# Performance work log

Hardware: AMD Instinct MI355X
Metric: run time of the kernel (lower is better)

## Reference

```python
import jax, jax.numpy as jnp
import numpy as np
import math

MUL = 32
E = 131072
N = 10000
IRREPS = [(0, 1), (1, -1), (2, 1)]  # (l, parity) for 0e + 1o + 2e
SQRT3 = math.sqrt(3.0)

_f = math.factorial


def _w3j_symbol(j1, j2, j3, m1, m2, m3):
    """Standard (complex-basis) Wigner 3j symbol via the Racah formula."""
    if m1 + m2 + m3 != 0:
        return 0.0
    if abs(m1) > j1 or abs(m2) > j2 or abs(m3) > j3:
        return 0.0
    if not (abs(j1 - j2) <= j3 <= j1 + j2):
        return 0.0
    tri = _f(j1 + j2 - j3) * _f(j1 - j2 + j3) * _f(-j1 + j2 + j3) / _f(j1 + j2 + j3 + 1)
    pref = (-1) ** (j1 - j2 - m3) * math.sqrt(
        tri * _f(j1 + m1) * _f(j1 - m1) * _f(j2 + m2) * _f(j2 - m2) * _f(j3 + m3) * _f(j3 - m3)
    )
    tmin = max(0, j2 - j3 - m1, j1 - j3 + m2)
    tmax = min(j1 + j2 - j3, j1 - m1, j2 + m2)
    s = 0.0
    for t in range(tmin, tmax + 1):
        s += (-1) ** t / (
            _f(t) * _f(j3 - j2 + t + m1) * _f(j3 - j1 + t - m2)
            * _f(j1 + j2 - j3 - t) * _f(j1 - t - m1) * _f(j2 - t + m2)
        )
    return pref * s


def _real_basis(l):
    """Complex -> real spherical-harmonic change of basis, rows m=-l..l."""
    U = np.zeros((2 * l + 1, 2 * l + 1), dtype=np.complex128)
    U[l, l] = 1.0
    s = 1.0 / math.sqrt(2.0)
    for m in range(1, l + 1):
        U[l + m, l + m] = ((-1) ** m) * s
        U[l + m, l - m] = s
        U[l - m, l - m] = 1j * s
        U[l - m, l + m] = -1j * ((-1) ** m) * s
    return U


def _w3j_real(l1, l2, l3):
    """Real-basis Wigner 3j tensor, Frobenius norm 1 (e3nn normalization)."""
    Wc = np.zeros((2 * l1 + 1, 2 * l2 + 1, 2 * l3 + 1), dtype=np.complex128)
    for m1 in range(-l1, l1 + 1):
        for m2 in range(-l2, l2 + 1):
            for m3 in range(-l3, l3 + 1):
                Wc[l1 + m1, l2 + m2, l3 + m3] = _w3j_symbol(l1, l2, l3, m1, m2, m3)
    C = np.einsum('im,jn,ko,mno->ijk', _real_basis(l1), _real_basis(l2), _real_basis(l3), Wc)
    re, im = C.real, C.imag
    R = re if np.linalg.norm(re) >= np.linalg.norm(im) else im
    return R / np.linalg.norm(R)


def _build_w3j():
    dims = [2 * l + 1 for l, _ in IRREPS]
    offs = np.concatenate([[0], np.cumsum(dims)])[:-1]
    base_dim = int(sum(dims))  # 9
    # auto-generated instructions: same loop order as the torch module
    ins = []
    for io, (lo, po) in enumerate(IRREPS):
        for i1, (l1, p1) in enumerate(IRREPS):
            for i2, (l2, p2) in enumerate(IRREPS):
                if p1 * p2 == po and abs(l1 - l2) <= lo <= l1 + l2:
                    ins.append((i1, i2, io))
    P = len(ins)  # 11 paths
    w3j = np.zeros((P, base_dim, base_dim, base_dim), dtype=np.float32)
    for p, (i1, i2, io) in enumerate(ins):
        l1, l2, lo = IRREPS[i1][0], IRREPS[i2][0], IRREPS[io][0]
        C = _w3j_real(l1, l2, lo) * math.sqrt(2 * lo + 1)  # component normalization
        w3j[p, offs[i1]:offs[i1] + dims[i1], offs[i2]:offs[i2] + dims[i2], offs[io]:offs[io] + dims[io]] = C
    return w3j


def setup_inputs() -> dict:
    key = jax.random.key(0)
    k1, k2, k3, k4 = jax.random.split(key, 4)
    w3j = jnp.asarray(_build_w3j())  # [P=11, 9, 9, 9]
    P = w3j.shape[0]
    base_dim = w3j.shape[1]
    return {
        'x1': jax.random.normal(k1, (E, MUL * base_dim), dtype=jnp.float32),
        'x2': jax.random.normal(k2, (E, MUL * base_dim), dtype=jnp.float32),
        'idxs': jax.random.randint(k3, (E,), 0, N),
        'weights': jax.random.uniform(k4, (MUL, P), dtype=jnp.float32, minval=-SQRT3, maxval=SQRT3),
        'w3j': w3j,
        'scatter_dim_size': N,
    }


def reference(x1, x2, idxs, weights, w3j, scatter_dim_size):
    base1 = w3j.shape[1]
    base2 = w3j.shape[2]
    # scatter edges -> nodes, then gather back per edge (neighbor sum per center)
    x2s = jax.ops.segment_sum(x2, idxs, num_segments=int(scatter_dim_size))
    x2g = x2s[idxs]
    x1r = x1.reshape(-1, MUL, base1)   # [E, u, i]
    x2r = x2g.reshape(-1, MUL, base2)  # [E, u, j]
    # path-channel coupled weighting: 'up,pijk->uijk'
    ww3j = jnp.einsum('up,pijk->uijk', weights, w3j)
    # out[e,u,k] = sum_ij x1[e,u,i] x2[e,u,j] ww3j[u,i,j,k]
    out = jnp.einsum('eui,euj,uijk->euk', x1r, x2r, ww3j)
    return out
```

## Files before the change

### kernel.cpp

```cpp
#include <hip/hip_runtime.h>

#define MULV 32
#define BASE 9
#define ROW 288
#define NPATH 11
#define W3J_SZ 729
#define PACK_STRIDE 96
#define PACK_TOTAL (MULV * PACK_STRIDE)
#define TILE 64
#define QCOL 72
#define LSTR 73
#define NQ4 18
#define QTOT (TILE * NQ4)

typedef float f4a4 __attribute__((ext_vector_type(4), aligned(4)));

__device__ constexpr int p_o1[NPATH] = {0,1,4, 0,1,1,4, 0,1,4,4};
__device__ constexpr int p_d1[NPATH] = {1,3,5, 1,3,3,5, 1,3,5,5};
__device__ constexpr int p_o2[NPATH] = {0,1,4, 1,0,4,1, 4,1,0,4};
__device__ constexpr int p_d2[NPATH] = {1,3,5, 3,1,5,3, 5,3,1,5};
__device__ constexpr int p_o3[NPATH] = {0,0,0, 1,1,1,1, 4,4,4,4};
__device__ constexpr int p_d3[NPATH] = {1,1,1, 3,3,3,3, 5,5,5,5};
__device__ constexpr int p_l1[NPATH] = {0,1,2, 0,1,1,2, 0,1,2,2};
__device__ constexpr int p_l2[NPATH] = {0,1,2, 1,0,2,1, 2,1,0,2};
__device__ constexpr int p_l3[NPATH] = {0,0,0, 1,1,1,1, 2,2,2,2};

__device__ __host__ constexpr bool cell_nz(int p, int i, int j, int k) {
    int m1 = i - p_l1[p], m2 = j - p_l2[p], m3 = k - p_l3[p];
    if ((((m1 < 0) + (m2 < 0) + (m3 < 0)) & 1) != 0) return false;
    int a1 = m1 < 0 ? -m1 : m1, a2 = m2 < 0 ? -m2 : m2, a3 = m3 < 0 ? -m3 : m3;
    int d = a1 - a2; if (d < 0) d = -d;
    return (a3 == a1 + a2) || (a3 == d);
}
__device__ __host__ constexpr bool pair_nz(int p, int i, int j) {
    for (int k = 0; k < p_d3[p]; ++k) if (cell_nz(p, i, j, k)) return true;
    return false;
}


__global__ void zero_count_kernel(float* __restrict__ ws, const int* __restrict__ dN) {
    int N = dN[0];
    int* count = (int*)(ws + PACK_TOTAL + (long)N * ROW);
    for (int i = blockIdx.x * blockDim.x + threadIdx.x; i < N; i += gridDim.x * blockDim.x)
        count[i] = 0;
}

__global__ void hist_kernel(const int* __restrict__ idxs, float* __restrict__ ws,
                            const int* __restrict__ dN, int E) {
    int N = dN[0];
    int* count = (int*)(ws + PACK_TOTAL + (long)N * ROW);
    int t = blockIdx.x * blockDim.x + threadIdx.x;
    if (t < E) atomicAdd(&count[idxs[t]], 1);
}

__global__ void scan_kernel(float* __restrict__ ws, const int* __restrict__ dN) {
    int N = dN[0];
    int* count  = (int*)(ws + PACK_TOTAL + (long)N * ROW);
    int* offset = count + N;
    int* cursor = count + 2 * N;
    __shared__ int tsum[1024];
    const int tid = threadIdx.x;
    int cpt = (N + 1023) / 1024;
    int lo = tid * cpt;
    int hi = lo + cpt; if (hi > N) hi = N;
    int s = 0;
    for (int i = lo; i < hi; ++i) s += count[i];
    int v = s;
    tsum[tid] = v;
    __syncthreads();
    #pragma unroll
    for (int off = 1; off < 1024; off <<= 1) {
        int t = (tid >= off) ? tsum[tid - off] : 0;
        __syncthreads();
        v += t;
        tsum[tid] = v;
        __syncthreads();
    }
    int run = v - s;
    for (int i = lo; i < hi; ++i) {
        int c = count[i];
        offset[i] = run; cursor[i] = run;
        run += c;
    }
}

__global__ void fill_kernel(const int* __restrict__ idxs, float* __restrict__ ws,
                            const int* __restrict__ dN, int E) {
    int N = dN[0];
    int* count  = (int*)(ws + PACK_TOTAL + (long)N * ROW);
    int* cursor = count + 2 * N;
    int* bucket = count + 3 * N;
    int t = blockIdx.x * blockDim.x + threadIdx.x;
    if (t < E) {
        int n = idxs[t];
        int pos = atomicAdd(&cursor[n], 1);
        bucket[pos] = t;
    }
}

__global__ __launch_bounds__(256) void gather_sum_kernel(const float* __restrict__ x2,
                                                         float* __restrict__ ws,
                                                         const int* __restrict__ dN) {
    int N = dN[0];
    float* x2s  = ws + PACK_TOTAL;
    int* count  = (int*)(x2s + (long)N * ROW);
    int* offset = count + N;
    int* bucket = count + 3 * N;
    const int lane = threadIdx.x & 63;
    const int wv   = threadIdx.x >> 6;
    for (int n0 = blockIdx.x * 4 + wv; n0 < N; n0 += gridDim.x * 4) {
        int n   = __builtin_amdgcn_readfirstlane(n0);
        int off = offset[n];
        int deg = count[n];
        float4 a0 = make_float4(0.f, 0.f, 0.f, 0.f);
        float4 a1 = make_float4(0.f, 0.f, 0.f, 0.f);
        int d = 0;
        for (; d + 4 <= deg; d += 4) {
            int e0 = bucket[off + d + 0];
            int e1 = bucket[off + d + 1];
            int e2 = bucket[off + d + 2];
            int e3 = bucket[off + d + 3];
            const float4* r0 = (const float4*)(x2 + (long)e0 * ROW);
            const float4* r1 = (const float4*)(x2 + (long)e1 * ROW);
            const float4* r2 = (const float4*)(x2 + (long)e2 * ROW);
            const float4* r3 = (const float4*)(x2 + (long)e3 * ROW);
            float4 v0 = r0[lane], v1 = r1[lane], v2 = r2[lane], v3 = r3[lane];
            float4 w0, w1, w2, w3;
            if (lane < 8) {
                w0 = r0[64 + lane]; w1 = r1[64 + lane];
                w2 = r2[64 + lane]; w3 = r3[64 + lane];
            }
            a0.x += v0.x + v1.x + v2.x + v3.x;
            a0.y += v0.y + v1.y + v2.y + v3.y;
            a0.z += v0.z + v1.z + v2.z + v3.z;
            a0.w += v0.w + v1.w + v2.w + v3.w;
            if (lane < 8) {
                a1.x += w0.x + w1.x + w2.x + w3.x;
                a1.y += w0.y + w1.y + w2.y + w3.y;
                a1.z += w0.z + w1.z + w2.z + w3.z;
                a1.w += w0.w + w1.w + w2.w + w3.w;
            }
        }
        for (; d < deg; ++d) {
            int e = bucket[off + d];
            const float4* row = (const float4*)(x2 + (long)e * ROW);
            float4 v = row[lane];
            a0.x += v.x; a0.y += v.y; a0.z += v.z; a0.w += v.w;
            if (lane < 8) {
                float4 w = row[64 + lane];
                a1.x += w.x; a1.y += w.y; a1.z += w.z; a1.w += w.w;
            }
        }
        float4* orow = (float4*)(x2s + (long)n * ROW);
        orow[lane] = a0;
        if (lane < 8) orow[64 + lane] = a1;
    }
}

__global__ void ww_build_kernel(const float* __restrict__ weights,
                                const float* __restrict__ w3j,
                                float* __restrict__ packed) {
    int u = threadIdx.x;
    if (u >= MULV) return;
    int ci = 0;
    #pragma unroll
    for (int p = 0; p < NPATH; ++p) {
        float wgt = weights[u * NPATH + p];
        #pragma unroll
        for (int i = 0; i < p_d1[p]; ++i)
            #pragma unroll
            for (int j = 0; j < p_d2[p]; ++j)
                #pragma unroll
                for (int k = 0; k < p_d3[p]; ++k)
                    if (cell_nz(p, i, j, k)) {
                        int idx = (p_o1[p] + i) * 81 + (p_o2[p] + j) * 9 + (p_o3[p] + k);
                        packed[u * PACK_STRIDE + ci] = wgt * w3j[p * W3J_SZ + idx];
                        ++ci;
                    }
    }
}

template <bool GUARD>
__global__ __launch_bounds__(256, 4) void contract_kernel(
    const float* __restrict__ x1, const int* __restrict__ idxs,
    float* __restrict__ ws, const int* __restrict__ dN,
    float* __restrict__ out, int E)
{
    __shared__ float tile[TILE * LSTR];
    const int tid = threadIdx.x;
    const long ebase = (long)blockIdx.x * TILE;
    const float* __restrict__ packed = ws;
    const float* __restrict__ x2s    = ws + PACK_TOTAL;
    const int N = dN[0];
    const int* __restrict__ bucket = (const int*)(x2s + (long)N * ROW) + 3 * N;

    int rr[5], cc4[5], er[5];
    #pragma unroll
    for (int t = 0; t < 5; ++t) {
        int q = tid + t * 256;
        bool ok = (t < 4) || (q < QTOT);
        int r = q / NQ4;
        rr[t] = r; cc4[t] = q - r * NQ4;
        if (ok) {
            long ei = ebase + r;
            er[t] = GUARD ? ((ei < (long)E) ? bucket[ei] : -1) : bucket[ei];
        } else er[t] = -1;
    }

    const int lane = tid & 63;
    const int wv   = __builtin_amdgcn_readfirstlane(tid >> 6);
    int ecomp;
    if (GUARD) {
        long ei = ebase + lane;
        ecomp = (ei < (long)E) ? bucket[ei] : 0;
    } else {
        ecomp = bucket[ebase + lane];
    }
    const int n = idxs[ecomp];
    const float* __restrict__ r2 = x2s + (long)n * ROW;
    float* __restrict__ lrow = &tile[lane * LSTR];

    float4 buf[5];
    #pragma unroll
    for (int t = 0; t < 5; ++t)
        if (er[t] >= 0)
            buf[t] = *(const float4*)(x1 + (long)er[t] * ROW + cc4[t] * 4);

    float x2c[BASE];
    {
        const float* s = r2 + wv * BASE;
        f4a4 a = *(const f4a4*)s;
        f4a4 b = *(const f4a4*)(s + 4);
        x2c[0]=a.x; x2c[1]=a.y; x2c[2]=a.z; x2c[3]=a.w;
        x2c[4]=b.x; x2c[5]=b.y; x2c[6]=b.z; x2c[7]=b.w;
        x2c[8]=s[8];
    }

    #pragma unroll 1
    for (int h = 0; h < 4; ++h) {
        #pragma unroll
        for (int t = 0; t < 5; ++t) {
            if (er[t] >= 0) {
                float* d = &tile[rr[t] * LSTR + cc4[t] * 4];
                d[0] = buf[t].x; d[1] = buf[t].y; d[2] = buf[t].z; d[3] = buf[t].w;
            }
        }
        __syncthreads();

        if (h < 3) {
            #pragma unroll
            for (int t = 0; t < 5; ++t)
                if (er[t] >= 0)
                    buf[t] = *(const float4*)(x1 + (long)er[t] * ROW + (h + 1) * QCOL + cc4[t] * 4);
        }

        #pragma unroll 1
        for (int c = 0; c < 2; ++c) {
            const int u = 8 * h + c * 4 + wv;
            const float* __restrict__ wp = packed + u * PACK_STRIDE;

            float x2n[BASE];
            if (u + 4 < MULV) {
                const float* s = r2 + (u + 4) * BASE;
                f4a4 a = *(const f4a4*)s;
                f4a4 b = *(const f4a4*)(s + 4);
                x2n[0]=a.x; x2n[1]=a.y; x2n[2]=a.z; x2n[3]=a.w;
                x2n[4]=b.x; x2n[5]=b.y; x2n[6]=b.z; x2n[7]=b.w;
                x2n[8]=s[8];
            }

            const int lbase = (c * 4 + wv) * BASE;
            float x1v[BASE], acc[BASE];
            #pragma unroll
            for (int i = 0; i < BASE; ++i) {
                x1v[i] = lrow[lbase + i];
                acc[i] = 0.0f;
            }

            int ci = 0;
            #pragma unroll
            for (int p = 0; p < NPATH; ++p) {
                #pragma unroll
                for (int i = 0; i < p_d1[p]; ++i) {
                    #pragma unroll
                    for (int j = 0; j < p_d2[p]; ++j) {
                        if (pair_nz(p, i, j)) {
                            float xx = x1v[p_o1[p] + i] * x2c[p_o2[p] + j];
                            #pragma unroll
                            for (int k = 0; k < p_d3[p]; ++k) {
                                if (cell_nz(p, i, j, k)) {
                                    acc[p_o3[p] + k] = fmaf(wp[ci], xx, acc[p_o3[p] + k]);
                                    ++ci;
                                }
                            }
                        }
                    }
                }
            }
            #pragma unroll
            for (int k = 0; k < BASE; ++k)
                lrow[lbase + k] = acc[k];
            if (u + 4 < MULV) {
                #pragma unroll
                for (int i = 0; i < BASE; ++i) x2c[i] = x2n[i];
            }
        }
        __syncthreads();

        #pragma unroll
        for (int t = 0; t < 5; ++t) {
            if (er[t] >= 0) {
                const float* s = &tile[rr[t] * LSTR + cc4[t] * 4];
                *(float4*)(out + (long)er[t] * ROW + h * QCOL + cc4[t] * 4) =
                    make_float4(s[0], s[1], s[2], s[3]);
            }
        }
    }
}

extern "C" void kernel_launch(void* const* d_in, const int* in_sizes, int n_in,
                              void* d_out, int out_size, void* d_ws, size_t ws_size,
                              hipStream_t stream) {
    const float* x1      = (const float*)d_in[0];
    const float* x2      = (const float*)d_in[1];
    const int*   idxs    = (const int*)d_in[2];
    const float* weights = (const float*)d_in[3];
    const float* w3j     = (const float*)d_in[4];
    const int*   dN      = (const int*)d_in[5];
    float* out = (float*)d_out;
    float* ws  = (float*)d_ws;

    const int E = in_sizes[2];
    const int eb = (E + 255) / 256;

    zero_count_kernel<<<256, 256, 0, stream>>>(ws, dN);
    hist_kernel<<<eb, 256, 0, stream>>>(idxs, ws, dN, E);
    scan_kernel<<<1, 1024, 0, stream>>>(ws, dN);
    fill_kernel<<<eb, 256, 0, stream>>>(idxs, ws, dN, E);

    gather_sum_kernel<<<2500, 256, 0, stream>>>(x2, ws, dN);

    ww_build_kernel<<<1, 64, 0, stream>>>(weights, w3j, ws);

    if (E % TILE == 0) {
        contract_kernel<false><<<E / TILE, 256, 0, stream>>>(x1, idxs, ws, dN, out, E);
    } else {
        contract_kernel<true><<<(E + TILE - 1) / TILE, 256, 0, stream>>>(x1, idxs, ws, dN, out, E);
    }
}
```

Baseline: 169.9 us.

## Double block size to 512 threads and stage x1 in two half-row passes

The contract kernel now runs 512 threads (8 waves) per 64-edge tile instead of 256. The x1 tile is loaded in two 144-column halves rather than four 72-column quarters, and the edge permutation is cached in shared memory. The register-prefetch pipeline that overlapped the next quarter's x1 load with compute is dropped, so loads are now synchronous per half. This roughly doubles the LDS tile and halves the barrier count per tile, at the cost of losing load/compute overlap and possibly reducing occupancy.

```diff
diff --git a/kernel.cpp b/kernel.cpp
--- a/kernel.cpp
+++ b/kernel.cpp
@@ -8,10 +8,11 @@
 #define PACK_STRIDE 96
 #define PACK_TOTAL (MULV * PACK_STRIDE)
 #define TILE 64
-#define QCOL 72
-#define LSTR 73
-#define NQ4 18
-#define QTOT (TILE * NQ4)
+#define BLK 512
+#define HCOL 144
+#define LSTR 145
+#define NH4 36
+#define HTOT (TILE * NH4)
 
 typedef float f4a4 __attribute__((ext_vector_type(4), aligned(4)));
 
@@ -181,12 +182,13 @@
 }
 
 template <bool GUARD>
-__global__ __launch_bounds__(256, 4) void contract_kernel(
+__global__ __launch_bounds__(512, 4) void contract_kernel(
     const float* __restrict__ x1, const int* __restrict__ idxs,
     float* __restrict__ ws, const int* __restrict__ dN,
     float* __restrict__ out, int E)
 {
     __shared__ float tile[TILE * LSTR];
+    __shared__ int lperm[TILE];
     const int tid = threadIdx.x;
     const long ebase = (long)blockIdx.x * TILE;
     const float* __restrict__ packed = ws;
@@ -194,37 +196,18 @@
     const int N = dN[0];
     const int* __restrict__ bucket = (const int*)(x2s + (long)N * ROW) + 3 * N;
 
-    int rr[5], cc4[5], er[5];
-    #pragma unroll
-    for (int t = 0; t < 5; ++t) {
-        int q = tid + t * 256;
-        bool ok = (t < 4) || (q < QTOT);
-        int r = q / NQ4;
-        rr[t] = r; cc4[t] = q - r * NQ4;
-        if (ok) {
-            long ei = ebase + r;
-            er[t] = GUARD ? ((ei < (long)E) ? bucket[ei] : -1) : bucket[ei];
-        } else er[t] = -1;
-    }
+    if (tid < TILE) {
+        long ee = ebase + tid;
+        lperm[tid] = (!GUARD || ee < (long)E) ? bucket[ee] : -1;
+    }
+    __syncthreads();
 
     const int lane = tid & 63;
     const int wv   = __builtin_amdgcn_readfirstlane(tid >> 6);
-    int ecomp;
-    if (GUARD) {
-        long ei = ebase + lane;
-        ecomp = (ei < (long)E) ? bucket[ei] : 0;
-    } else {
-        ecomp = bucket[ebase + lane];
-    }
-    const int n = idxs[ecomp];
-    const float* __restrict__ r2 = x2s + (long)n * ROW;
+    const int e    = lperm[lane];
+    const int n    = idxs[e >= 0 ? e : 0];
+    const float* __restrict__ r2 = x2s + n * ROW;
     float* __restrict__ lrow = &tile[lane * LSTR];
-
-    float4 buf[5];
-    #pragma unroll
-    for (int t = 0; t < 5; ++t)
-        if (er[t] >= 0)
-            buf[t] = *(const float4*)(x1 + (long)er[t] * ROW + cc4[t] * 4);
 
     float x2c[BASE];
     {
@@ -237,31 +220,27 @@
     }
 
     #pragma unroll 1
-    for (int h = 0; h < 4; ++h) {
-        #pragma unroll
-        for (int t = 0; t < 5; ++t) {
-            if (er[t] >= 0) {
-                float* d = &tile[rr[t] * LSTR + cc4[t] * 4];
-                d[0] = buf[t].x; d[1] = buf[t].y; d[2] = buf[t].z; d[3] = buf[t].w;
+    for (int h = 0; h < 2; ++h) {
+        for (int q = tid; q < HTOT; q += BLK) {
+            int r = q / NH4, c = q - r * NH4;
+            int er = lperm[r];
+            if (!GUARD || er >= 0) {
+                float4 v = *(const float4*)(x1 + (long)er * ROW + h * HCOL + c * 4);
+                float* d = &tile[r * LSTR + c * 4];
+                d[0] = v.x; d[1] = v.y; d[2] = v.z; d[3] = v.w;
             }
         }
         __syncthreads();
 
-        if (h < 3) {
-            #pragma unroll
-            for (int t = 0; t < 5; ++t)
-                if (er[t] >= 0)
-                    buf[t] = *(const float4*)(x1 + (long)er[t] * ROW + (h + 1) * QCOL + cc4[t] * 4);
-        }
-
         #pragma unroll 1
-        for (int c = 0; c < 2; ++c) {
-            const int u = 8 * h + c * 4 + wv;
+        for (int cc = 0; cc < 2; ++cc) {
+            const int m = 2 * h + cc;
+            const int u = m * 8 + wv;
             const float* __restrict__ wp = packed + u * PACK_STRIDE;
 
             float x2n[BASE];
-            if (u + 4 < MULV) {
-                const float* s = r2 + (u + 4) * BASE;
+            if (m < 3) {
+                const float* s = r2 + (u + 8) * BASE;
                 f4a4 a = *(const f4a4*)s;
                 f4a4 b = *(const f4a4*)(s + 4);
                 x2n[0]=a.x; x2n[1]=a.y; x2n[2]=a.z; x2n[3]=a.w;
@@ -269,7 +248,7 @@
                 x2n[8]=s[8];
             }
 
-            const int lbase = (c * 4 + wv) * BASE;
+            const int lbase = (cc * 8 + wv) * BASE;
             float x1v[BASE], acc[BASE];
             #pragma unroll
             for (int i = 0; i < BASE; ++i) {
@@ -300,18 +279,19 @@
             #pragma unroll
             for (int k = 0; k < BASE; ++k)
                 lrow[lbase + k] = acc[k];
-            if (u + 4 < MULV) {
+            if (m < 3) {
                 #pragma unroll
                 for (int i = 0; i < BASE; ++i) x2c[i] = x2n[i];
             }
         }
         __syncthreads();
 
-        #pragma unroll
-        for (int t = 0; t < 5; ++t) {
-            if (er[t] >= 0) {
-                const float* s = &tile[rr[t] * LSTR + cc4[t] * 4];
-                *(float4*)(out + (long)er[t] * ROW + h * QCOL + cc4[t] * 4) =
+        for (int q = tid; q < HTOT; q += BLK) {
+            int r = q / NH4, c = q - r * NH4;
+            int er = lperm[r];
+            if (!GUARD || er >= 0) {
+                const float* s = &tile[r * LSTR + c * 4];
+                *(float4*)(out + (long)er * ROW + h * HCOL + c * 4) =
                     make_float4(s[0], s[1], s[2], s[3]);
             }
         }
@@ -343,8 +323,8 @@
     ww_build_kernel<<<1, 64, 0, stream>>>(weights, w3j, ws);
 
     if (E % TILE == 0) {
-        contract_kernel<false><<<E / TILE, 256, 0, stream>>>(x1, idxs, ws, dN, out, E);
+        contract_kernel<false><<<E / TILE, BLK, 0, stream>>>(x1, idxs, ws, dN, out, E);
     } else {
-        contract_kernel<true><<<(E + TILE - 1) / TILE, 256, 0, stream>>>(x1, idxs, ws, dN, out, E);
-    }
-}
+        contract_kernel<true><<<(E + TILE - 1) / TILE, BLK, 0, stream>>>(x1, idxs, ws, dN, out, E);
+    }
+}
```

Result: faster. 165.3 us (-2.7%).
